# Kernel optimization log

Measured on AMD Instinct MI355X. Metric: run time of the kernel, lower is better.

The kernel has to match this reference:

```python
import jax, jax.numpy as jnp
import numpy as np

TAU = 0.5    # __init__ tau
ALPHA = 1.0  # __init__ alpha
T_PARAM = 1.0  # self.T (non-trainable, ones)


def setup_inputs() -> dict:
    key = jax.random.key(0)
    k1, k2, k3 = jax.random.split(key, 3)
    B, C, H, W = 4, 64, 512, 512
    x = jax.random.normal(k1, (B, C, H, W), dtype=jnp.float32)
    # mirror torch init: xavier W, eig(W @ W.T) -> real eigenbasis Q, Qinv = inv(Q)
    Wm = jax.random.normal(k2, (C, C), dtype=jnp.float32) * float(np.sqrt(1.0 / C))
    M = Wm @ Wm.T  # symmetric PSD -> real eigendecomposition
    _, Q = jnp.linalg.eigh(M)
    Qinv = jnp.linalg.inv(Q)
    # trainable eigenvalue vector S (torch inits to ones; random positive here)
    S = jax.random.uniform(k3, (C,), dtype=jnp.float32, minval=0.1, maxval=1.1)
    return {"x": x, "S": S, "Q": Q, "Qinv": Qinv, "T": 5}


def reference(x, S, Q, Qinv, T):
    # Delta = (1/tau) * -1 * |S|**alpha   (passed to ExpDecay as its 'Delta')
    Delta = -(1.0 / TAU) * jnp.abs(S) ** ALPHA  # [C]
    # F.linear(x.permute(0,2,3,1), Q).permute(0,3,1,2)  ==  einsum over channel dim
    z = jnp.einsum('bchw,fc->bfhw', x, Q)
    # ExpDecay.step: diag(exp(T_total * Delta)) applied as elementwise channel scale
    t_total = T_PARAM * float(T)
    z2 = z * jnp.exp(t_total * Delta)[None, :, None, None]
    # F.linear(..., Qinv) back-projection
    return jnp.einsum('bchw,fc->bfhw', z2, Qinv)
```

## Files before the change

### kernel.cpp

```cpp
#include <hip/hip_runtime.h>
#include <hip/hip_bf16.h>
#include <math.h>


#define C_DIM 64
#define HW (512 * 512)
#define CHUNK 16

__global__ __launch_bounds__(256) void compute_M_kernel(
    const float* __restrict__ S, const float* __restrict__ Q,
    const float* __restrict__ Qinv, const int* __restrict__ Tp,
    float* __restrict__ M) {
    __shared__ float d[C_DIM];
    int tid = threadIdx.x;
    if (tid < C_DIM) {
        float t = (float)(*Tp);
        d[tid] = expf(-2.0f * t * fabsf(S[tid]));
    }
    __syncthreads();
    int gid = blockIdx.x * blockDim.x + tid;
    int f = gid >> 6;
    int k = gid & 63;
    float acc = 0.0f;
    #pragma unroll
    for (int c = 0; c < C_DIM; ++c) {
        acc = fmaf(Qinv[f * C_DIM + c] * d[c], Q[c * C_DIM + k], acc);
    }
    M[gid] = acc;
}

__global__ __launch_bounds__(256, 4) void apply_M_kernel(
    const float* __restrict__ x, const float* __restrict__ M,
    float* __restrict__ out) {
    int t = blockIdx.x * 256 + threadIdx.x;
    int b = t >> 18;
    int s = t & (HW - 1);

    const float* xp = x + ((size_t)b * C_DIM) * HW + s;
    float*       op = out + ((size_t)b * C_DIM) * HW + s;

    float acc[C_DIM];
    #pragma unroll
    for (int f = 0; f < C_DIM; ++f) acc[f] = 0.0f;

    float xv[CHUNK], xn[CHUNK];
    #pragma unroll
    for (int c = 0; c < CHUNK; ++c) xv[c] = xp[(size_t)c * HW];

    #pragma unroll
    for (int chunk = 0; chunk < C_DIM / CHUNK; ++chunk) {
        if (chunk < C_DIM / CHUNK - 1) {
            #pragma unroll
            for (int c = 0; c < CHUNK; ++c)
                xn[c] = xp[(size_t)((chunk + 1) * CHUNK + c) * HW];
        }
        #pragma unroll
        for (int f = 0; f < C_DIM; ++f) {
            float a = acc[f];
            #pragma unroll
            for (int c = 0; c < CHUNK; ++c)
                a = fmaf(M[f * C_DIM + chunk * CHUNK + c], xv[c], a);
            acc[f] = a;
        }
        #pragma unroll
        for (int c = 0; c < CHUNK; ++c) xv[c] = xn[c];
    }

    #pragma unroll
    for (int f = 0; f < C_DIM; ++f) op[(size_t)f * HW] = acc[f];
}

extern "C" void kernel_launch(void* const* d_in, const int* in_sizes, int n_in,
                              void* d_out, int out_size, void* d_ws, size_t ws_size,
                              hipStream_t stream) {
    const float* x    = (const float*)d_in[0];
    const float* S    = (const float*)d_in[1];
    const float* Q    = (const float*)d_in[2];
    const float* Qinv = (const float*)d_in[3];
    const int*   Tp   = (const int*)d_in[4];
    float* out = (float*)d_out;
    float* M = (float*)d_ws;

    compute_M_kernel<<<16, 256, 0, stream>>>(S, Q, Qinv, Tp, M);

    apply_M_kernel<<<(4 * HW) / 256, 256, 0, stream>>>(x, M, out);
}
```

Before: 524.0 us.

## Compute channel mix with bf16x3 split MFMA instead of scalar FMAs

```diff
diff --git a/kernel.cpp b/kernel.cpp
--- a/kernel.cpp
+++ b/kernel.cpp
@@ -5,12 +5,23 @@
 
 #define C_DIM 64
 #define HW (512 * 512)
-#define CHUNK 16
+
+typedef __attribute__((ext_vector_type(8))) short short8;
+typedef __attribute__((ext_vector_type(4))) float float4v;
+
+__device__ inline unsigned short f32_to_bf16_rne(float f) {
+    unsigned int u = __float_as_uint(f);
+    unsigned int r = (u + 0x7fffu + ((u >> 16) & 1u)) >> 16;
+    return (unsigned short)r;
+}
+__device__ inline float bf16_to_f32(unsigned short h) {
+    return __uint_as_float(((unsigned int)h) << 16);
+}
 
 __global__ __launch_bounds__(256) void compute_M_kernel(
     const float* __restrict__ S, const float* __restrict__ Q,
     const float* __restrict__ Qinv, const int* __restrict__ Tp,
-    float* __restrict__ M) {
+    unsigned short* __restrict__ Mh, unsigned short* __restrict__ Ml) {
     __shared__ float d[C_DIM];
     int tid = threadIdx.x;
     if (tid < C_DIM) {
@@ -18,7 +29,7 @@
         d[tid] = expf(-2.0f * t * fabsf(S[tid]));
     }
     __syncthreads();
-    int gid = blockIdx.x * blockDim.x + tid;
+    int gid = blockIdx.x * 256 + tid;
     int f = gid >> 6;
     int k = gid & 63;
     float acc = 0.0f;
@@ -26,48 +37,74 @@
     for (int c = 0; c < C_DIM; ++c) {
         acc = fmaf(Qinv[f * C_DIM + c] * d[c], Q[c * C_DIM + k], acc);
     }
-    M[gid] = acc;
+    unsigned short h = f32_to_bf16_rne(acc);
+    Mh[gid] = h;
+    Ml[gid] = f32_to_bf16_rne(acc - bf16_to_f32(h));
 }
 
-__global__ __launch_bounds__(256, 4) void apply_M_kernel(
-    const float* __restrict__ x, const float* __restrict__ M,
-    float* __restrict__ out) {
-    int t = blockIdx.x * 256 + threadIdx.x;
-    int b = t >> 18;
-    int s = t & (HW - 1);
+__global__ __launch_bounds__(256) void apply_M_mfma(
+    const float* __restrict__ x, const unsigned short* __restrict__ Mh,
+    const unsigned short* __restrict__ Ml, float* __restrict__ out) {
+    int lane = threadIdx.x & 63;
+    int wid = (blockIdx.x * 256 + threadIdx.x) >> 6;
+    int n  = lane & 15;
+    int kg = lane >> 4;
 
-    const float* xp = x + ((size_t)b * C_DIM) * HW + s;
-    float*       op = out + ((size_t)b * C_DIM) * HW + s;
+    long long px0 = (long long)wid * 16;
+    int b = (int)(px0 >> 18);
+    int s = (int)(px0 & (HW - 1));
 
-    float acc[C_DIM];
+    const float* xb = x   + (size_t)b * C_DIM * HW + s + n;
+    float*       ob = out + (size_t)b * C_DIM * HW + s + n;
+
+    float xf[2][8];
     #pragma unroll
-    for (int f = 0; f < C_DIM; ++f) acc[f] = 0.0f;
+    for (int kt = 0; kt < 2; ++kt) {
+        #pragma unroll
+        for (int j = 0; j < 8; ++j) {
+            int c = kt * 32 + kg * 8 + j;
+            xf[kt][j] = xb[(size_t)c * HW];
+        }
+    }
 
-    float xv[CHUNK], xn[CHUNK];
+    short8 Bh[2], Bl[2];
     #pragma unroll
-    for (int c = 0; c < CHUNK; ++c) xv[c] = xp[(size_t)c * HW];
+    for (int kt = 0; kt < 2; ++kt) {
+        #pragma unroll
+        for (int j = 0; j < 8; ++j) {
+            float v = xf[kt][j];
+            unsigned short h = f32_to_bf16_rne(v);
+            float rem = v - bf16_to_f32(h);
+            Bh[kt][j] = (short)h;
+            Bl[kt][j] = (short)f32_to_bf16_rne(rem);
+        }
+    }
+
+    float4v acc[4];
+    #pragma unroll
+    for (int ft = 0; ft < 4; ++ft) acc[ft] = (float4v){0.f, 0.f, 0.f, 0.f};
 
     #pragma unroll
-    for (int chunk = 0; chunk < C_DIM / CHUNK; ++chunk) {
-        if (chunk < C_DIM / CHUNK - 1) {
-            #pragma unroll
-            for (int c = 0; c < CHUNK; ++c)
-                xn[c] = xp[(size_t)((chunk + 1) * CHUNK + c) * HW];
+    for (int ft = 0; ft < 4; ++ft) {
+        #pragma unroll
+        for (int kt = 0; kt < 2; ++kt) {
+            size_t aoff = (size_t)(ft * 16 + n) * C_DIM + kt * 32 + kg * 8;
+            short8 ah = *reinterpret_cast<const short8*>(Mh + aoff);
+            short8 al = *reinterpret_cast<const short8*>(Ml + aoff);
+            acc[ft] = __builtin_amdgcn_mfma_f32_16x16x32_bf16(ah, Bh[kt], acc[ft], 0, 0, 0);
+            acc[ft] = __builtin_amdgcn_mfma_f32_16x16x32_bf16(ah, Bl[kt], acc[ft], 0, 0, 0);
+            acc[ft] = __builtin_amdgcn_mfma_f32_16x16x32_bf16(al, Bh[kt], acc[ft], 0, 0, 0);
         }
-        #pragma unroll
-        for (int f = 0; f < C_DIM; ++f) {
-            float a = acc[f];
-            #pragma unroll
-            for (int c = 0; c < CHUNK; ++c)
-                a = fmaf(M[f * C_DIM + chunk * CHUNK + c], xv[c], a);
-            acc[f] = a;
-        }
-        #pragma unroll
-        for (int c = 0; c < CHUNK; ++c) xv[c] = xn[c];
     }
 
     #pragma unroll
-    for (int f = 0; f < C_DIM; ++f) op[(size_t)f * HW] = acc[f];
+    for (int ft = 0; ft < 4; ++ft) {
+        #pragma unroll
+        for (int r = 0; r < 4; ++r) {
+            int f = ft * 16 + kg * 4 + r;
+            ob[(size_t)f * HW] = acc[ft][r];
+        }
+    }
 }
 
 extern "C" void kernel_launch(void* const* d_in, const int* in_sizes, int n_in,
@@ -79,9 +116,12 @@
     const float* Qinv = (const float*)d_in[3];
     const int*   Tp   = (const int*)d_in[4];
     float* out = (float*)d_out;
-    float* M = (float*)d_ws;
 
-    compute_M_kernel<<<16, 256, 0, stream>>>(S, Q, Qinv, Tp, M);
+    unsigned short* Mh = (unsigned short*)d_ws;
+    unsigned short* Ml = Mh + C_DIM * C_DIM;
 
-    apply_M_kernel<<<(4 * HW) / 256, 256, 0, stream>>>(x, M, out);
+    compute_M_kernel<<<16, 256, 0, stream>>>(S, Q, Qinv, Tp, Mh, Ml);
+
+    int total_waves = (4 * HW) / 16;
+    apply_M_mfma<<<total_waves / 4, 256, 0, stream>>>(x, Mh, Ml, out);
 }
```

New measurement: 539.4 us. +2.9%, slower.
